# Kernel tuning notes

Hardware: AMD Instinct MI355X
Metric: run time of the kernel (lower is better)

## Reference

```python
import jax, jax.numpy as jnp
import numpy as np

NUM_EXPERTS = 8
TOP_K = 2


def setup_inputs() -> dict:
    key = jax.random.key(0)
    ks = jax.random.split(key, 6)
    B, S, D, H, E = 4, 1024, 1024, 2048, NUM_EXPERTS
    x = jax.random.normal(ks[0], (B, S, D), dtype=jnp.float32)
    Wg = jax.random.normal(ks[1], (D, E), dtype=jnp.float32) * 0.02
    W1 = jax.random.normal(ks[2], (E, D, H), dtype=jnp.float32) * 0.02
    b1 = jax.random.normal(ks[3], (E, H), dtype=jnp.float32) * 0.02
    W2 = jax.random.normal(ks[4], (E, H, D), dtype=jnp.float32) * 0.02
    b2 = jax.random.normal(ks[5], (E, D), dtype=jnp.float32) * 0.02
    return {"x": x, "Wg": Wg, "W1": W1, "b1": b1, "W2": W2, "b2": b2}


def reference(x, Wg, W1, b1, W2, b2):
    B, S, D = x.shape
    E, _, H = W1.shape
    OUT = W2.shape[2]
    xm = x.reshape(-1, D)                      # [N, D], N = B*S
    # --- top-k gating (ProbabilitySamplerTopk): softmax over experts, take top-k ---
    logits = xm @ Wg                           # [N, E]
    probs = jax.nn.softmax(logits, axis=-1)
    topk_p, topk_i = jax.lax.top_k(probs, TOP_K)   # [N, K]
    # --- sort dispatched (token, expert) pairs by expert id (stable) ---
    flat_e = topk_i.reshape(-1)                # [N*K]
    flat_p = topk_p.reshape(-1)                # [N*K]
    order = jnp.argsort(flat_e)                # stable sort -> grouped by expert
    tok_idx = order // TOP_K                   # source token index (trunc-div by topK)
    e_sorted = flat_e[order]                   # [N*K]
    p_sorted = flat_p[order]                   # [N*K]
    xs = xm[tok_idx]                           # [N*K, D] expert-sorted inputs
    # --- grouped-GEMM experts: masked per-expert dense GEMM (E is small & fixed) ---
    y = jnp.zeros((xs.shape[0], OUT), dtype=xs.dtype)
    for e in range(E):
        h = jax.nn.relu(xs @ W1[e] + b1[e])    # [N*K, H]
        ye = h @ W2[e] + b2[e]                 # [N*K, OUT]
        m = (e_sorted == e)[:, None].astype(xs.dtype)
        y = y + m * ye
    # --- combine: multiply by gates, scatter-add back to token slots ---
    y = y * p_sorted[:, None]
    out = jnp.zeros((B * S, OUT), dtype=y.dtype).at[tok_idx].add(y)
    return out.reshape(B, S, OUT)
```

## Files before the change

### kernel.cpp

```cpp
#include <hip/hip_runtime.h>
#include <hip/hip_bf16.h>
#include <stdint.h>

typedef __bf16 bf16;
typedef __bf16 bf16x8 __attribute__((ext_vector_type(8)));
typedef __bf16 bf16x4 __attribute__((ext_vector_type(4)));
typedef float f32x4 __attribute__((ext_vector_type(4)));

#define N_TOK 4096
#define DDIM 1024
#define HDIM 2048
#define NPAIR 8192
#define BM 256
#define BN 128
#define BK 32
#define MTILES 39

__device__ __forceinline__ void gload16(const void* g, void* l) {
  __builtin_amdgcn_global_load_lds(
      (const __attribute__((address_space(1))) unsigned int*)g,
      (__attribute__((address_space(3))) unsigned int*)l, 16, 0, 0);
}

__global__ void transpose_cvt_kernel(const float* __restrict__ in, bf16* __restrict__ out,
                                     int R, int C) {
  __shared__ float tile[32][33];
  const float* ip = in + (size_t)blockIdx.z * R * C;
  bf16* op = out + (size_t)blockIdx.z * R * C;
  int r0 = blockIdx.y * 32, c0 = blockIdx.x * 32;
  int tr = threadIdx.x >> 3;
  int tc = (threadIdx.x & 7) * 4;
  float4 v = *(const float4*)(ip + (size_t)(r0 + tr) * C + c0 + tc);
  tile[tr][tc] = v.x; tile[tr][tc + 1] = v.y; tile[tr][tc + 2] = v.z; tile[tr][tc + 3] = v.w;
  __syncthreads();
  bf16x4 o = {(bf16)tile[tc + 0][tr], (bf16)tile[tc + 1][tr],
              (bf16)tile[tc + 2][tr], (bf16)tile[tc + 3][tr]};
  *(bf16x4*)(op + (size_t)(c0 + tr) * R + r0 + tc) = o;
}

__global__ void gate_kernel(const float* __restrict__ x, const float* __restrict__ Wg,
                            int2* __restrict__ ge, float2* __restrict__ gp,
                            bf16* __restrict__ xb) {
  int t = blockIdx.x * 4 + (threadIdx.x >> 6);
  int lane = threadIdx.x & 63;
  const float* xr = x + (size_t)t * DDIM;
  bf16* xbr = xb + (size_t)t * DDIM;
  float a[8];
#pragma unroll
  for (int e = 0; e < 8; e++) a[e] = 0.f;
#pragma unroll
  for (int it = 0; it < 4; it++) {
    int d0 = it * 256 + lane * 4;
    float4 xv = *(const float4*)(xr + d0);
    bf16x4 o = {(bf16)xv.x, (bf16)xv.y, (bf16)xv.z, (bf16)xv.w};
    *(bf16x4*)(xbr + d0) = o;
    float xs[4] = {xv.x, xv.y, xv.z, xv.w};
#pragma unroll
    for (int dd = 0; dd < 4; dd++) {
      float4 w0 = *(const float4*)(Wg + (size_t)(d0 + dd) * 8);
      float4 w1 = *(const float4*)(Wg + (size_t)(d0 + dd) * 8 + 4);
      a[0] += xs[dd] * w0.x; a[1] += xs[dd] * w0.y; a[2] += xs[dd] * w0.z; a[3] += xs[dd] * w0.w;
      a[4] += xs[dd] * w1.x; a[5] += xs[dd] * w1.y; a[6] += xs[dd] * w1.z; a[7] += xs[dd] * w1.w;
    }
  }
#pragma unroll
  for (int off = 32; off >= 1; off >>= 1) {
#pragma unroll
    for (int e = 0; e < 8; e++) a[e] += __shfl_xor(a[e], off);
  }
  if (lane == 0) {
    float m = a[0];
#pragma unroll
    for (int e = 1; e < 8; e++) m = fmaxf(m, a[e]);
    float p[8]; float s = 0.f;
#pragma unroll
    for (int e = 0; e < 8; e++) { p[e] = expf(a[e] - m); s += p[e]; }
    float inv = 1.f / s;
    int i0 = 0; float v0 = a[0];
#pragma unroll
    for (int e = 1; e < 8; e++) if (a[e] > v0) { v0 = a[e]; i0 = e; }
    int i1 = -1; float v1 = -1e30f;
#pragma unroll
    for (int e = 0; e < 8; e++) if (e != i0 && a[e] > v1) { v1 = a[e]; i1 = e; }
    ge[t] = make_int2(i0, i1);
    gp[t] = make_float2(p[i0] * inv, p[i1] * inv);
  }
}

__global__ void sort_kernel(const int2* __restrict__ ge, const float2* __restrict__ gp,
                            int* __restrict__ tok, float* __restrict__ ps,
                            int* __restrict__ meta) {
  __shared__ int hist[8], runn[8], wc[16][8], wb[16][8], baseS[9];
  int tid = threadIdx.x;
  int lane = tid & 63, wv = tid >> 6;
  if (tid < 8) hist[tid] = 0;
  __syncthreads();
  for (int i = tid; i < NPAIR; i += 1024) {
    int2 g = ge[i >> 1];
    int e = (i & 1) ? g.y : g.x;
    atomicAdd(&hist[e], 1);
  }
  __syncthreads();
  if (tid == 0) {
    int b = 0, ts = 0;
    for (int e = 0; e < 8; e++) {
      baseS[e] = b; meta[e] = b; meta[9 + e] = ts;
      b += hist[e]; ts += (hist[e] + BM - 1) / BM;
    }
    baseS[8] = b; meta[8] = b; meta[17] = ts;
  }
  __syncthreads();
  if (tid < 8) runn[tid] = baseS[tid];
  __syncthreads();
  for (int c = 0; c < 8; c++) {
    int i = c * 1024 + tid;
    int2 g = ge[i >> 1];
    int e = (i & 1) ? g.y : g.x;
    int rank = 0;
#pragma unroll
    for (int ee = 0; ee < 8; ee++) {
      unsigned long long b = __ballot(e == ee);
      if (e == ee) rank = __popcll(b & ((1ull << lane) - 1ull));
      if (lane == 0) wc[wv][ee] = __popcll(b);
    }
    __syncthreads();
    if (tid < 8) {
      int s = runn[tid];
      for (int w = 0; w < 16; w++) { wb[w][tid] = s; s += wc[w][tid]; }
      runn[tid] = s;
    }
    __syncthreads();
    int pos = wb[wv][e] + rank;
    tok[pos] = i >> 1;
    float2 p2 = gp[i >> 1];
    ps[pos] = (i & 1) ? p2.y : p2.x;
    __syncthreads();
  }
}

__global__ void zero_kernel(float4* __restrict__ p) {
  p[blockIdx.x * 256 + threadIdx.x] = make_float4(0.f, 0.f, 0.f, 0.f);
}

template <int KDIM, int NPE, bool FIRST>
__global__ __launch_bounds__(512, 4)
void moe_gemm_kernel(const bf16* __restrict__ A, const bf16* __restrict__ Bt,
                     const float* __restrict__ bias, const int* __restrict__ tok,
                     const float* __restrict__ ps, const int* __restrict__ meta,
                     bf16* __restrict__ hout, float* __restrict__ outp, int MT) {
  __shared__ bf16 lds[3][12288];

  int nwg = gridDim.x;
  int orig = blockIdx.x;
  int q = nwg >> 3, rr8 = nwg & 7;
  int xcd = orig & 7, off8 = orig >> 3;
  int lin = (xcd < rr8 ? xcd * (q + 1) : rr8 * (q + 1) + (xcd - rr8) * q) + off8;
  int tileN = lin / MT;
  int tileM = lin - tileN * MT;
  if (tileM >= meta[17]) return;
  int e = 0;
#pragma unroll
  for (int k = 1; k < 8; k++) if (tileM >= meta[9 + k]) e = k;
  int row0 = meta[e] + (tileM - meta[9 + e]) * BM;
  int segEnd = meta[e + 1];
  int n0 = tileN * BN;

  int t = threadIdx.x;
  const bf16* aSrc[2];
  const bf16* bSrc;
  {
    int swz = ((t & 3) ^ ((t >> 3) & 3)) * 8;
#pragma unroll
    for (int r = 0; r < 2; r++) {
      int row = r * 128 + (t >> 2);
      int gRow = row0 + row; if (gRow > NPAIR - 1) gRow = NPAIR - 1;
      int arow = FIRST ? tok[gRow] : gRow;
      aSrc[r] = A + (size_t)arow * KDIM + swz;
    }
    bSrc = Bt + ((size_t)e * NPE + n0 + (t >> 2)) * KDIM + swz;
  }

  int lane = t & 63, wv = t >> 6;
  int wm = wv >> 1, wn = wv & 1;
  int l15 = lane & 15, l4 = lane >> 4;
  int aOff[4], bOff[4];
#pragma unroll
  for (int m = 0; m < 4; m++) {
    int row = wm * 64 + m * 16 + l15;
    aOff[m] = row * 32 + ((l4 ^ ((row >> 1) & 3)) * 8);
  }
#pragma unroll
  for (int n = 0; n < 4; n++) {
    int row = wn * 64 + n * 16 + l15;
    bOff[n] = 8192 + row * 32 + ((l4 ^ ((row >> 1) & 3)) * 8);
  }

  f32x4 acc[4][4];
#pragma unroll
  for (int m = 0; m < 4; m++)
#pragma unroll
    for (int n = 0; n < 4; n++)
#pragma unroll
      for (int j = 0; j < 4; j++) acc[m][n][j] = 0.f;

  auto STAGE = [&](int kt, int slot) {
    bf16* sb = &lds[slot][0];
    int ko = kt * BK;
    gload16(aSrc[0] + ko, sb + t * 8);
    gload16(aSrc[1] + ko, sb + 4096 + t * 8);
    gload16(bSrc + ko, sb + 8192 + t * 8);
  };

  constexpr int nk = KDIM / BK;
  STAGE(0, 0);
  STAGE(1, 1);
  for (int kt = 0; kt < nk; kt++) {
    if (kt == nk - 1) asm volatile("s_waitcnt vmcnt(0)\n\ts_barrier" ::: "memory");
    else              asm volatile("s_waitcnt vmcnt(3)\n\ts_barrier" ::: "memory");
    if (kt + 2 < nk) STAGE(kt + 2, (kt + 2) % 3);
    __builtin_amdgcn_sched_barrier(0);
    const bf16* sb = &lds[kt % 3][0];
    bf16x8 af[4], bfr[4];
#pragma unroll
    for (int m = 0; m < 4; m++) af[m] = *(const bf16x8*)(sb + aOff[m]);
#pragma unroll
    for (int n = 0; n < 4; n++) bfr[n] = *(const bf16x8*)(sb + bOff[n]);
    __builtin_amdgcn_s_setprio(1);
#pragma unroll
    for (int m = 0; m < 4; m++)
#pragma unroll
      for (int n = 0; n < 4; n++)
        acc[m][n] = __builtin_amdgcn_mfma_f32_16x16x32_bf16(af[m], bfr[n], acc[m][n], 0, 0, 0);
    __builtin_amdgcn_s_setprio(0);
  }

  int colb = n0 + wn * 64 + l15;
  int rowb = wm * 64 + l4 * 4;
  float bia[4];
#pragma unroll
  for (int n = 0; n < 4; n++) bia[n] = bias[(size_t)e * NPE + colb + n * 16];
#pragma unroll
  for (int m = 0; m < 4; m++) {
#pragma unroll
    for (int j = 0; j < 4; j++) {
      int gRow = row0 + rowb + m * 16 + j;
      if (gRow < segEnd) {
        if (FIRST) {
#pragma unroll
          for (int n = 0; n < 4; n++) {
            float v = acc[m][n][j] + bia[n];
            v = fmaxf(v, 0.f);
            hout[(size_t)gRow * NPE + colb + n * 16] = (bf16)v;
          }
        } else {
          float pscale = ps[gRow];
          float* orow = outp + (size_t)tok[gRow] * DDIM;
#pragma unroll
          for (int n = 0; n < 4; n++) {
            float v = (acc[m][n][j] + bia[n]) * pscale;
            atomicAdd(orow + colb + n * 16, v);
          }
        }
      }
    }
  }
}

extern "C" void kernel_launch(void* const* d_in, const int* in_sizes, int n_in,
                              void* d_out, int out_size, void* d_ws, size_t ws_size,
                              hipStream_t stream) {
  (void)in_sizes; (void)n_in; (void)ws_size;
  const float* x  = (const float*)d_in[0];
  const float* Wg = (const float*)d_in[1];
  const float* W1 = (const float*)d_in[2];
  const float* b1 = (const float*)d_in[3];
  const float* W2 = (const float*)d_in[4];
  const float* b2 = (const float*)d_in[5];
  float* out = (float*)d_out;

  char* ws = (char*)d_ws;
  bf16*  xb   = (bf16*)(ws);
  bf16*  W1T  = (bf16*)(ws + (8ull  << 20));
  bf16*  W2T  = (bf16*)(ws + (40ull << 20));
  bf16*  hbuf = (bf16*)(ws + (72ull << 20));
  char*  ext  = ws + (104ull << 20);
  int2*   ge      = (int2*)(ext);
  float2* gp      = (float2*)(ext + (64u  << 10));
  int*    tok     = (int*)(ext + (128u << 10));
  float*  psarr   = (float*)(ext + (160u << 10));
  int*    meta    = (int*)(ext + (224u << 10));

  transpose_cvt_kernel<<<dim3(64, 32, 8), 256, 0, stream>>>(W1, W1T, 1024, 2048);
  transpose_cvt_kernel<<<dim3(32, 64, 8), 256, 0, stream>>>(W2, W2T, 2048, 1024);
  gate_kernel<<<1024, 256, 0, stream>>>(x, Wg, ge, gp, xb);
  sort_kernel<<<1, 1024, 0, stream>>>(ge, gp, tok, psarr, meta);
  zero_kernel<<<out_size / 1024, 256, 0, stream>>>((float4*)out);
  moe_gemm_kernel<1024, 2048, true><<<dim3(MTILES * 16), 512, 0, stream>>>(
      xb, W1T, b1, tok, psarr, meta, hbuf, nullptr, MTILES);
  moe_gemm_kernel<2048, 1024, false><<<dim3(MTILES * 8), 512, 0, stream>>>(
      hbuf, W2T, b2, tok, psarr, meta, nullptr, out, MTILES);
}
```

Measured before the change: 219.1 us.

## Use 128-row tiles for first expert GEMM and XCD-contiguous tile mapping

The first grouped GEMM now uses 128-row M tiles with 256-thread blocks, while the second keeps 256-row tiles. The sort kernel emits tile prefix tables for both tile heights. Block-to-tile mapping now hands each XCD a contiguous M-tile range and exits surplus blocks, replacing the earlier remap. Smaller tiles are meant to cut padding waste on partial per-expert tiles and give more blocks for load balance. In exchange, each tile reuses loaded B data less and more blocks launch.

```diff
diff --git a/kernel.cpp b/kernel.cpp
--- a/kernel.cpp
+++ b/kernel.cpp
@@ -11,10 +11,8 @@
 #define DDIM 1024
 #define HDIM 2048
 #define NPAIR 8192
-#define BM 256
-#define BN 128
-#define BK 32
-#define MTILES 39
+#define MT128 71
+#define MT256 39
 
 __device__ __forceinline__ void gload16(const void* g, void* l) {
   __builtin_amdgcn_global_load_lds(
@@ -102,12 +100,14 @@
   }
   __syncthreads();
   if (tid == 0) {
-    int b = 0, ts = 0;
+    int b = 0, ts1 = 0, ts2 = 0;
     for (int e = 0; e < 8; e++) {
-      baseS[e] = b; meta[e] = b; meta[9 + e] = ts;
-      b += hist[e]; ts += (hist[e] + BM - 1) / BM;
-    }
-    baseS[8] = b; meta[8] = b; meta[17] = ts;
+      baseS[e] = b; meta[e] = b;
+      meta[9 + e] = ts1;  ts1 += (hist[e] + 127) / 128;
+      meta[18 + e] = ts2; ts2 += (hist[e] + 255) / 256;
+      b += hist[e];
+    }
+    baseS[8] = b; meta[8] = b; meta[17] = ts1; meta[26] = ts2;
   }
   __syncthreads();
   if (tid < 8) runn[tid] = baseS[tid];
@@ -142,42 +142,51 @@
   p[blockIdx.x * 256 + threadIdx.x] = make_float4(0.f, 0.f, 0.f, 0.f);
 }
 
-template <int KDIM, int NPE, bool FIRST>
-__global__ __launch_bounds__(512, 4)
+template <int KDIM, int NPE, bool FIRST, int BMT, int THREADS, int NT, int MAPOFF>
+__global__ __launch_bounds__(THREADS, (THREADS == 256) ? 3 : 4)
 void moe_gemm_kernel(const bf16* __restrict__ A, const bf16* __restrict__ Bt,
                      const float* __restrict__ bias, const int* __restrict__ tok,
                      const float* __restrict__ ps, const int* __restrict__ meta,
-                     bf16* __restrict__ hout, float* __restrict__ outp, int MT) {
-  __shared__ bf16 lds[3][12288];
-
-  int nwg = gridDim.x;
-  int orig = blockIdx.x;
-  int q = nwg >> 3, rr8 = nwg & 7;
-  int xcd = orig & 7, off8 = orig >> 3;
-  int lin = (xcd < rr8 ? xcd * (q + 1) : rr8 * (q + 1) + (xcd - rr8) * q) + off8;
-  int tileN = lin / MT;
-  int tileM = lin - tileN * MT;
-  if (tileM >= meta[17]) return;
+                     bf16* __restrict__ hout, float* __restrict__ outp) {
+  constexpr int AR = BMT * 4 / THREADS;
+  constexpr int BR = 128 * 4 / THREADS;
+  constexpr int SLOT = (BMT + 128) * 32;
+  __shared__ bf16 lds[3][SLOT];
+
+  int MTa = meta[MAPOFF + 8];
+  int xcd = blockIdx.x & 7;
+  int idx = blockIdx.x >> 3;
+  int mLo = (MTa * xcd) >> 3;
+  int mHi = (MTa * (xcd + 1)) >> 3;
+  int cnt = mHi - mLo;
+  if (idx >= cnt * NT) return;
+  int tileN = idx / cnt;
+  int tileM = mLo + idx - tileN * cnt;
+
   int e = 0;
 #pragma unroll
-  for (int k = 1; k < 8; k++) if (tileM >= meta[9 + k]) e = k;
-  int row0 = meta[e] + (tileM - meta[9 + e]) * BM;
+  for (int k = 1; k < 8; k++) if (tileM >= meta[MAPOFF + k]) e = k;
+  int row0 = meta[e] + (tileM - meta[MAPOFF + e]) * BMT;
   int segEnd = meta[e + 1];
-  int n0 = tileN * BN;
+  int n0 = tileN * 128;
 
   int t = threadIdx.x;
-  const bf16* aSrc[2];
-  const bf16* bSrc;
+  const bf16* aSrc[AR];
+  const bf16* bSrc[BR];
   {
     int swz = ((t & 3) ^ ((t >> 3) & 3)) * 8;
 #pragma unroll
-    for (int r = 0; r < 2; r++) {
-      int row = r * 128 + (t >> 2);
+    for (int r = 0; r < AR; r++) {
+      int row = r * (THREADS / 4) + (t >> 2);
       int gRow = row0 + row; if (gRow > NPAIR - 1) gRow = NPAIR - 1;
       int arow = FIRST ? tok[gRow] : gRow;
       aSrc[r] = A + (size_t)arow * KDIM + swz;
     }
-    bSrc = Bt + ((size_t)e * NPE + n0 + (t >> 2)) * KDIM + swz;
+#pragma unroll
+    for (int r = 0; r < BR; r++) {
+      int row = r * (THREADS / 4) + (t >> 2);
+      bSrc[r] = Bt + ((size_t)e * NPE + n0 + row) * KDIM + swz;
+    }
   }
 
   int lane = t & 63, wv = t >> 6;
@@ -192,7 +201,7 @@
 #pragma unroll
   for (int n = 0; n < 4; n++) {
     int row = wn * 64 + n * 16 + l15;
-    bOff[n] = 8192 + row * 32 + ((l4 ^ ((row >> 1) & 3)) * 8);
+    bOff[n] = BMT * 32 + row * 32 + ((l4 ^ ((row >> 1) & 3)) * 8);
   }
 
   f32x4 acc[4][4];
@@ -205,18 +214,20 @@
 
   auto STAGE = [&](int kt, int slot) {
     bf16* sb = &lds[slot][0];
-    int ko = kt * BK;
-    gload16(aSrc[0] + ko, sb + t * 8);
-    gload16(aSrc[1] + ko, sb + 4096 + t * 8);
-    gload16(bSrc + ko, sb + 8192 + t * 8);
+    int ko = kt * 32;
+#pragma unroll
+    for (int r = 0; r < AR; r++) gload16(aSrc[r] + ko, sb + (r * THREADS + t) * 8);
+#pragma unroll
+    for (int r = 0; r < BR; r++) gload16(bSrc[r] + ko, sb + BMT * 32 + (r * THREADS + t) * 8);
   };
 
-  constexpr int nk = KDIM / BK;
+  constexpr int nk = KDIM / 32;
   STAGE(0, 0);
   STAGE(1, 1);
   for (int kt = 0; kt < nk; kt++) {
     if (kt == nk - 1) asm volatile("s_waitcnt vmcnt(0)\n\ts_barrier" ::: "memory");
-    else              asm volatile("s_waitcnt vmcnt(3)\n\ts_barrier" ::: "memory");
+    else if constexpr (AR + BR == 4) asm volatile("s_waitcnt vmcnt(4)\n\ts_barrier" ::: "memory");
+    else                             asm volatile("s_waitcnt vmcnt(3)\n\ts_barrier" ::: "memory");
     if (kt + 2 < nk) STAGE(kt + 2, (kt + 2) % 3);
     __builtin_amdgcn_sched_barrier(0);
     const bf16* sb = &lds[kt % 3][0];
@@ -295,8 +306,8 @@
   gate_kernel<<<1024, 256, 0, stream>>>(x, Wg, ge, gp, xb);
   sort_kernel<<<1, 1024, 0, stream>>>(ge, gp, tok, psarr, meta);
   zero_kernel<<<out_size / 1024, 256, 0, stream>>>((float4*)out);
-  moe_gemm_kernel<1024, 2048, true><<<dim3(MTILES * 16), 512, 0, stream>>>(
-      xb, W1T, b1, tok, psarr, meta, hbuf, nullptr, MTILES);
-  moe_gemm_kernel<2048, 1024, false><<<dim3(MTILES * 8), 512, 0, stream>>>(
-      hbuf, W2T, b2, tok, psarr, meta, nullptr, out, MTILES);
-}
+  moe_gemm_kernel<1024, 2048, true, 128, 256, 16, 9><<<dim3(1152), 256, 0, stream>>>(
+      xb, W1T, b1, tok, psarr, meta, hbuf, nullptr);
+  moe_gemm_kernel<2048, 1024, false, 256, 512, 8, 18><<<dim3(320), 512, 0, stream>>>(
+      hbuf, W2T, b2, tok, psarr, meta, nullptr, out);
+}
```

Result: faster. 201.4 us (-8.1%).
